# Performance work log

Hardware: AMD Instinct MI355X
Metric: run time of the kernel (lower is better)

The kernel has to match this reference:

```python
import jax, jax.numpy as jnp
import numpy as np

B, N, R = 2, 16384, 2048
CA, CS, CP, H = 128, 256, 16, 4
WQ, WK = 32, 128
NW = N // WQ
CH = CA // H
INF = 1e8


def _ln(x, w=None, b=None, eps=1e-5):
    m = jnp.mean(x, axis=-1, keepdims=True)
    v = jnp.var(x, axis=-1, keepdims=True)
    y = (x - m) * jax.lax.rsqrt(v + eps)
    if w is not None:
        y = y * w
    if b is not None:
        y = y + b
    return y


def _gather_res(x, idx):
    # x: [B, R, C], idx: [B, N] -> [B, N, C]  (torch.gather dim=1)
    return jnp.take_along_axis(x, idx[..., None], axis=1)


def _adaln(s, cond, idx, ln_w, Wg, bg, Wb):
    s = _ln(s)                      # LayerNorm, no affine
    cond = _ln(cond, ln_w)          # LayerNorm, weight only
    gate = _gather_res(cond @ Wg + bg, idx)
    bias = _gather_res(cond @ Wb, idx)
    return s * jax.nn.sigmoid(gate) + bias


def setup_inputs():
    key = jax.random.key(0)
    ks = jax.random.split(key, 20)

    def nrm(k, shape, scale=0.02):
        return jax.random.normal(k, shape, jnp.float32) * scale

    # key-window validity mask (keys are wk-wide windows centered on each wq query window)
    centers = np.arange(NW) * WQ + WQ // 2
    kidx = centers[:, None] - WK // 2 + np.arange(WK)[None, :]
    valid = (kidx >= 0) & (kidx < N)                              # [NW, WK]
    atompair_mask = jnp.broadcast_to(jnp.asarray(valid)[None, :, None, :], (B, NW, WQ, WK))

    return dict(
        atom_features=jax.random.normal(ks[0], (B, N, CA), jnp.float32),
        res_features=jax.random.normal(ks[1], (B, R, CS), jnp.float32),
        atompair_features=jax.random.normal(ks[2], (B, NW, WQ, WK, CP), jnp.float32),
        atom_res_idx=jnp.sort(jax.random.randint(ks[3], (B, N), 0, R), axis=1),
        atompos_mask=jnp.ones((B, N), jnp.float32),
        atompair_mask=atompair_mask,
        # attention AdaLN
        a_ln_w=jnp.ones((CS,), jnp.float32),
        a_Wg=nrm(ks[4], (CS, CA)), a_bg=jnp.zeros((CA,), jnp.float32), a_Wb=nrm(ks[5], (CS, CA)),
        # q / kv projections
        q_W=nrm(ks[6], (CA, CA)), q_b=jnp.zeros((CA,), jnp.float32), kv_W=nrm(ks[7], (CA, 2 * CA)),
        # pair bias head: LayerNorm(c_atompair) + Linear(c_atompair -> H, no bias)
        bij_ln_w=jnp.ones((CP,), jnp.float32), bij_ln_b=jnp.zeros((CP,), jnp.float32), bij_W=nrm(ks[8], (CP, H)),
        # residue-conditioned output gate (bias init -2)
        sg_W=nrm(ks[9], (CS, CA)), sg_b=jnp.full((CA,), -2.0, jnp.float32),
        # transition AdaLN + SwiGLU + cond gate
        t_ln_w=jnp.ones((CS,), jnp.float32),
        t_Wg=nrm(ks[10], (CS, CA)), t_bg=jnp.zeros((CA,), jnp.float32), t_Wb=nrm(ks[11], (CS, CA)),
        t_W1=nrm(ks[12], (CA, 2 * CA)), t_W2=nrm(ks[13], (CA, 2 * CA)),
        t_Wc=nrm(ks[14], (CS, CA)), t_bc=jnp.full((CA,), -2.0, jnp.float32),
        t_Wo=nrm(ks[15], (2 * CA, CA)),
    )


def reference(atom_features, res_features, atompair_features, atom_res_idx,
              atompos_mask, atompair_mask,
              a_ln_w, a_Wg, a_bg, a_Wb,
              q_W, q_b, kv_W,
              bij_ln_w, bij_ln_b, bij_W,
              sg_W, sg_b,
              t_ln_w, t_Wg, t_bg, t_Wb,
              t_W1, t_W2, t_Wc, t_bc, t_Wo):
    B_, N_ = atom_features.shape[0], atom_features.shape[1]
    # to_keys index: wk-wide key window centered on each query window (clamped; mask handles edges)
    centers = jnp.arange(NW) * WQ + WQ // 2
    kidx = jnp.clip(centers[:, None] - WK // 2 + jnp.arange(WK)[None, :], 0, N_ - 1)  # [NW, WK]

    # --- attention ---
    s = _adaln(atom_features, res_features, atom_res_idx, a_ln_w, a_Wg, a_bg, a_Wb)
    q = (s @ q_W + q_b).reshape(B_, NW, WQ, H, CH)                 # to_queries + unflatten
    kv = jnp.take(s @ kv_W, kidx, axis=1)                          # to_keys -> [B, NW, WK, 2*CA]
    kv = kv.reshape(B_, NW, WK, 2 * H, CH)
    k, v = kv[..., :H, :], kv[..., H:, :]
    a = jnp.einsum('bnqhc,bnkhc->bnqkh', q, k) / np.sqrt(CH)
    b_ij = _ln(atompair_features, bij_ln_w, bij_ln_b) @ bij_W      # [B, NW, WQ, WK, H]
    a = a + b_ij - INF * (1.0 - atompair_mask.astype(a.dtype)[..., None])
    p = jax.nn.softmax(a, axis=3)                                  # softmax over keys
    attn_out = jnp.einsum('bnqkh,bnkhc->bnqhc', p, v).reshape(B_, N_, CA)
    gate = jax.nn.sigmoid(res_features @ sg_W + sg_b)              # raw res_features (no LN)
    attn_out = attn_out * _gather_res(gate, atom_res_idx)

    atom = atom_features + attn_out * atompos_mask[..., None]

    # --- gather-conditioned transition ---
    t = _adaln(atom, res_features, atom_res_idx, t_ln_w, t_Wg, t_bg, t_Wb)
    b = jax.nn.silu(t @ t_W1) * (t @ t_W2)                          # SwiGLU, n=2
    tg = jax.nn.sigmoid(_gather_res(res_features @ t_Wc + t_bc, atom_res_idx))
    trans = tg * (b @ t_Wo)

    return atom + trans * atompos_mask[..., None]
```

## Files before the change

### kernel.cpp

```cpp
#include <hip/hip_runtime.h>
#include <hip/hip_bf16.h>
#include <string.h>

namespace {

constexpr int Bc  = 2;
constexpr int Nc  = 16384;
constexpr int Rc  = 2048;
constexpr int CAc = 128;
constexpr int CSc = 256;
constexpr int CPc = 16;
constexpr int Hc  = 4;
constexpr int WQc = 32;
constexpr int WKc = 128;
constexpr int NWc = 512;
constexpr float EPSf     = 1e-5f;
constexpr float NEG_INF  = -1e8f;
constexpr float QK_SCALE = 0.17677669529663687f;

constexpr int VT_STRIDE = 16512;
constexpr int VT_BATCH  = 128 * VT_STRIDE;

typedef short bf16x8 __attribute__((ext_vector_type(8)));
typedef float f32x4 __attribute__((ext_vector_type(4)));
typedef unsigned int u32x4 __attribute__((ext_vector_type(4)));

__device__ __forceinline__ float wsum(float v) {
#pragma unroll
  for (int m = 1; m < 64; m <<= 1) v += __shfl_xor(v, m, 64);
  return v;
}
__device__ __forceinline__ float sigm(float x) { return 1.0f / (1.0f + __expf(-x)); }
__device__ __forceinline__ float f4c(const float4& v, int i) {
  return i == 0 ? v.x : i == 1 ? v.y : i == 2 ? v.z : v.w;
}
__device__ __forceinline__ unsigned short bfx(float v) {
  __hip_bfloat16 h = __float2bfloat16(v);
  unsigned short u;
  memcpy(&u, &h, 2);
  return u;
}
__device__ __forceinline__ unsigned pk2(float a, float b) {
  return (unsigned)bfx(a) | ((unsigned)bfx(b) << 16);
}
__device__ __forceinline__ float ubf(unsigned us) {
  unsigned v = us << 16;
  float f;
  memcpy(&f, &v, 4);
  return f;
}
__device__ __forceinline__ bf16x8 ldfrag(const ushort* p) {
  return __builtin_bit_cast(bf16x8, *(const u32x4*)p);
}

__global__ void k_pack(const float* __restrict__ q_W, const float* __restrict__ kv_W,
                       const float* __restrict__ t_W1, const float* __restrict__ t_W2,
                       const float* __restrict__ t_Wo,
                       ushort* __restrict__ qWt, ushort* __restrict__ kvWt,
                       ushort* __restrict__ midWt, ushort* __restrict__ WoT,
                       ushort* __restrict__ vT) {
  const int i = blockIdx.x * 256 + threadIdx.x;
  if (i < 16384) {
    const int n = i >> 7, k = i & 127;
    qWt[i] = bfx(q_W[k * 128 + n]);
  } else if (i < 49152) {
    const int i2 = i - 16384;
    const int n = i2 >> 7, k = i2 & 127;
    kvWt[i2] = bfx(kv_W[k * 256 + n]);
  } else if (i < 114688) {
    const int i3 = i - 49152;
    const int n = i3 >> 7, k = i3 & 127;
    midWt[i3] = bfx(n < 256 ? t_W1[k * 256 + n] : t_W2[k * 256 + (n - 256)]);
  } else if (i < 147456) {
    const int i4 = i - 114688;
    const int n = i4 >> 8, k = i4 & 255;
    WoT[i4] = bfx(t_Wo[k * 128 + n]);
  } else if (i < 180224) {
    const int j = i - 147456;
    const int b = j >> 14, rem = j & 16383;
    const int d = rem >> 7, p = rem & 127;
    const int col = (p < 64) ? p : (16384 + p);
    vT[(size_t)b * VT_BATCH + (size_t)d * VT_STRIDE + col] = 0;
  }
}

__global__ void k_res_ln(const float* __restrict__ res, const float* __restrict__ a_ln_w,
                         const float* __restrict__ t_ln_w, float* __restrict__ lnA,
                         float* __restrict__ lnT) {
  const int wid = threadIdx.x >> 6, lane = threadIdx.x & 63;
  const int row = blockIdx.x * 4 + wid;
  const float* r = res + (size_t)row * CSc;
  float x[4], s = 0.f, sq = 0.f;
#pragma unroll
  for (int i = 0; i < 4; ++i) { x[i] = r[lane + 64 * i]; s += x[i]; sq += x[i] * x[i]; }
  s = wsum(s); sq = wsum(sq);
  const float mn = s * (1.0f / CSc);
  const float var = sq * (1.0f / CSc) - mn * mn;
  const float rs = rsqrtf(var + EPSf);
#pragma unroll
  for (int i = 0; i < 4; ++i) {
    const int c = lane + 64 * i;
    const float y = (x[i] - mn) * rs;
    lnA[(size_t)row * CSc + c] = y * a_ln_w[c];
    lnT[(size_t)row * CSc + c] = y * t_ln_w[c];
  }
}

__global__ void k_res_gemm(const float* __restrict__ lnA, const float* __restrict__ lnT,
                           const float* __restrict__ res,
                           const float* __restrict__ a_Wg, const float* __restrict__ a_bg,
                           const float* __restrict__ a_Wb,
                           const float* __restrict__ t_Wg, const float* __restrict__ t_bg,
                           const float* __restrict__ t_Wb,
                           const float* __restrict__ sg_W, const float* __restrict__ sg_b,
                           const float* __restrict__ t_Wc, const float* __restrict__ t_bc,
                           float* __restrict__ Ag, float* __restrict__ Ab,
                           float* __restrict__ Tg, float* __restrict__ Tb,
                           float* __restrict__ Sg, float* __restrict__ Tc) {
  __shared__ float tile[32 * CSc];
  const int m = blockIdx.y;
  const float* in = (m < 2) ? lnA : (m < 4) ? lnT : res;
  const float* W  = (m == 0) ? a_Wg : (m == 1) ? a_Wb : (m == 2) ? t_Wg
                  : (m == 3) ? t_Wb : (m == 4) ? sg_W : t_Wc;
  const float* bias = (m == 0) ? a_bg : (m == 2) ? t_bg : (m == 4) ? sg_b
                    : (m == 5) ? t_bc : nullptr;
  const bool sig = (m == 0) || (m == 2) || (m == 4) || (m == 5);
  float* out = (m == 0) ? Ag : (m == 1) ? Ab : (m == 2) ? Tg
             : (m == 3) ? Tb : (m == 4) ? Sg : Tc;
  const int row0 = blockIdx.x * 32;
  const float4* src = (const float4*)(in + (size_t)row0 * CSc);
  float4* dst = (float4*)tile;
#pragma unroll
  for (int k = 0; k < 8; ++k) dst[threadIdx.x + 256 * k] = src[threadIdx.x + 256 * k];
  __syncthreads();
  const int c0 = (threadIdx.x & 31) * 4;
  const int r0 = (threadIdx.x >> 5) * 4;
  float acc[4][4] = {};
  for (int j = 0; j < CSc; j += 4) {
    float4 a[4];
#pragma unroll
    for (int r = 0; r < 4; ++r) a[r] = *(const float4*)&tile[(r0 + r) * CSc + j];
#pragma unroll
    for (int jj = 0; jj < 4; ++jj) {
      const float4 w = *(const float4*)&W[(size_t)(j + jj) * CAc + c0];
#pragma unroll
      for (int r = 0; r < 4; ++r) {
        const float av = f4c(a[r], jj);
        acc[r][0] += av * w.x; acc[r][1] += av * w.y;
        acc[r][2] += av * w.z; acc[r][3] += av * w.w;
      }
    }
  }
  float4 bv = make_float4(0.f, 0.f, 0.f, 0.f);
  if (bias) bv = *(const float4*)&bias[c0];
#pragma unroll
  for (int r = 0; r < 4; ++r) {
    float4 o;
    o.x = acc[r][0] + bv.x; o.y = acc[r][1] + bv.y;
    o.z = acc[r][2] + bv.z; o.w = acc[r][3] + bv.w;
    if (sig) { o.x = sigm(o.x); o.y = sigm(o.y); o.z = sigm(o.z); o.w = sigm(o.w); }
    *(float4*)&out[(size_t)(row0 + r0 + r) * CAc + c0] = o;
  }
}

__global__ void k_adaln16(const float* __restrict__ in, const int* __restrict__ idxG,
                          const float* __restrict__ G, const float* __restrict__ Bb,
                          unsigned* __restrict__ out32) {
  const int wid = threadIdx.x >> 6, lane = threadIdx.x & 63;
  const int row = blockIdx.x * 4 + wid;
  const int b = row >> 14;
  const float* r = in + (size_t)row * CAc;
  const float2 xp = *(const float2*)&r[2 * lane];
  const float s = wsum(xp.x + xp.y);
  const float sq = wsum(xp.x * xp.x + xp.y * xp.y);
  const float mn = s * (1.0f / CAc);
  const float var = sq * (1.0f / CAc) - mn * mn;
  const float rs = rsqrtf(var + EPSf);
  const int base = (b * Rc + idxG[row]) * CAc;
  const float2 g2 = *(const float2*)&G[base + 2 * lane];
  const float2 b2 = *(const float2*)&Bb[base + 2 * lane];
  const float y0 = (xp.x - mn) * rs * g2.x + b2.x;
  const float y1 = (xp.y - mn) * rs * g2.y + b2.y;
  out32[(size_t)row * 64 + lane] = pk2(y0, y1);
}

__global__ __launch_bounds__(256) void k_gemm_qkv(
    const ushort* __restrict__ act16, const ushort* __restrict__ qWt,
    const ushort* __restrict__ kvWt, const float* __restrict__ q_b,
    ushort* __restrict__ q16, ushort* __restrict__ k16, ushort* __restrict__ vT) {
  __shared__ ushort vtile[128][72];
  const int ny = blockIdx.y;
  const int wid = threadIdx.x >> 6, lane = threadIdx.x & 63;
  const int c = lane & 15, s = lane >> 4;
  const int wm = wid & 1, wn = wid >> 1;
  const int base = blockIdx.x * 64;
  const int m0 = base + wm * 32;
  const int nb = wn * 64;
  const ushort* Wt = (ny == 0) ? qWt : kvWt + (ny == 2 ? 128 * 128 : 0);
  f32x4 acc[4][2];
#pragma unroll
  for (int nt = 0; nt < 4; ++nt)
#pragma unroll
    for (int mt = 0; mt < 2; ++mt) { acc[nt][mt][0]=0.f; acc[nt][mt][1]=0.f; acc[nt][mt][2]=0.f; acc[nt][mt][3]=0.f; }
#pragma unroll
  for (int kk = 0; kk < 4; ++kk) {
    const int k0 = kk * 32 + 8 * s;
    bf16x8 bA[2];
#pragma unroll
    for (int mt = 0; mt < 2; ++mt)
      bA[mt] = ldfrag(&act16[(size_t)(m0 + mt * 16 + c) * 128 + k0]);
#pragma unroll
    for (int nt = 0; nt < 4; ++nt) {
      const bf16x8 aW = ldfrag(&Wt[(size_t)(nb + nt * 16 + c) * 128 + k0]);
#pragma unroll
      for (int mt = 0; mt < 2; ++mt)
        acc[nt][mt] = __builtin_amdgcn_mfma_f32_16x16x32_bf16(aW, bA[mt], acc[nt][mt], 0, 0, 0);
    }
  }
#pragma unroll
  for (int nt = 0; nt < 4; ++nt) {
    const int colb = nb + nt * 16 + 4 * s;
    float4 qb4 = make_float4(0.f, 0.f, 0.f, 0.f);
    if (ny == 0) qb4 = *(const float4*)&q_b[colb];
#pragma unroll
    for (int mt = 0; mt < 2; ++mt) {
      const int m = m0 + mt * 16 + c;
      const f32x4 a = acc[nt][mt];
      if (ny == 0) {
        ushort4 u4;
        u4.x = bfx((a[0] + qb4.x) * QK_SCALE); u4.y = bfx((a[1] + qb4.y) * QK_SCALE);
        u4.z = bfx((a[2] + qb4.z) * QK_SCALE); u4.w = bfx((a[3] + qb4.w) * QK_SCALE);
        *(ushort4*)&q16[(size_t)m * 128 + colb] = u4;
      } else if (ny == 1) {
        ushort4 u4;
        u4.x = bfx(a[0]); u4.y = bfx(a[1]); u4.z = bfx(a[2]); u4.w = bfx(a[3]);
        *(ushort4*)&k16[(size_t)m * 128 + colb] = u4;
      } else {
        const int rowl = wm * 32 + mt * 16 + c;
#pragma unroll
        for (int r = 0; r < 4; ++r)
          vtile[colb + r][rowl] = bfx(a[r]);
      }
    }
  }
  if (ny == 2) {
    __syncthreads();
    const int bb = base >> 14, nn0 = base & 16383;
    const int t = threadIdx.x;
    const int d = t >> 1, half = t & 1;
    ushort* dst = vT + (size_t)bb * VT_BATCH + (size_t)d * VT_STRIDE + 64 + nn0 + half * 32;
    const ushort* srcl = &vtile[d][half * 32];
#pragma unroll
    for (int u = 0; u < 4; ++u)
      *(uint4*)(dst + u * 8) = *(const uint4*)(srcl + u * 8);
  }
}

__global__ __launch_bounds__(256) void k_gemm_mid(
    const ushort* __restrict__ act16, const ushort* __restrict__ midWt,
    ushort* __restrict__ bmid16) {
  const int wid = threadIdx.x >> 6, lane = threadIdx.x & 63;
  const int c = lane & 15, s = lane >> 4;
  const int wm = wid & 1, wn = wid >> 1;
  const int m0 = blockIdx.x * 64 + wm * 32;
  const int nb = blockIdx.y * 64 + wn * 32;
  f32x4 acc1[2][2], acc2[2][2];
#pragma unroll
  for (int nt = 0; nt < 2; ++nt)
#pragma unroll
    for (int mt = 0; mt < 2; ++mt) {
      acc1[nt][mt][0]=0.f; acc1[nt][mt][1]=0.f; acc1[nt][mt][2]=0.f; acc1[nt][mt][3]=0.f;
      acc2[nt][mt][0]=0.f; acc2[nt][mt][1]=0.f; acc2[nt][mt][2]=0.f; acc2[nt][mt][3]=0.f;
    }
#pragma unroll
  for (int kk = 0; kk < 4; ++kk) {
    const int k0 = kk * 32 + 8 * s;
    bf16x8 bA[2];
#pragma unroll
    for (int mt = 0; mt < 2; ++mt)
      bA[mt] = ldfrag(&act16[(size_t)(m0 + mt * 16 + c) * 128 + k0]);
#pragma unroll
    for (int nt = 0; nt < 2; ++nt) {
      const bf16x8 aW1 = ldfrag(&midWt[(size_t)(nb + nt * 16 + c) * 128 + k0]);
      const bf16x8 aW2 = ldfrag(&midWt[(size_t)(256 + nb + nt * 16 + c) * 128 + k0]);
#pragma unroll
      for (int mt = 0; mt < 2; ++mt) {
        acc1[nt][mt] = __builtin_amdgcn_mfma_f32_16x16x32_bf16(aW1, bA[mt], acc1[nt][mt], 0, 0, 0);
        acc2[nt][mt] = __builtin_amdgcn_mfma_f32_16x16x32_bf16(aW2, bA[mt], acc2[nt][mt], 0, 0, 0);
      }
    }
  }
#pragma unroll
  for (int nt = 0; nt < 2; ++nt) {
    const int colb = nb + nt * 16 + 4 * s;
#pragma unroll
    for (int mt = 0; mt < 2; ++mt) {
      const int m = m0 + mt * 16 + c;
      ushort4 u4;
#pragma unroll
      for (int r = 0; r < 4; ++r) {
        const float a1 = acc1[nt][mt][r];
        const float v = a1 * sigm(a1) * acc2[nt][mt][r];
        ((unsigned short*)&u4)[r] = bfx(v);
      }
      *(ushort4*)&bmid16[(size_t)m * 256 + colb] = u4;
    }
  }
}

__global__ __launch_bounds__(256) void k_gemm_out(
    const ushort* __restrict__ bmid16, const ushort* __restrict__ WoT,
    const float* __restrict__ atomw, const int* __restrict__ idxG,
    const float* __restrict__ TcG, const float* __restrict__ pmask,
    float* __restrict__ outG) {
  const int wid = threadIdx.x >> 6, lane = threadIdx.x & 63;
  const int c = lane & 15, s = lane >> 4;
  const int wm = wid & 1, wn = wid >> 1;
  const int m0 = blockIdx.x * 64 + wm * 32;
  const int nb = wn * 64;
  f32x4 acc[4][2];
#pragma unroll
  for (int nt = 0; nt < 4; ++nt)
#pragma unroll
    for (int mt = 0; mt < 2; ++mt) { acc[nt][mt][0]=0.f; acc[nt][mt][1]=0.f; acc[nt][mt][2]=0.f; acc[nt][mt][3]=0.f; }
#pragma unroll
  for (int kk = 0; kk < 8; ++kk) {
    const int k0 = kk * 32 + 8 * s;
    bf16x8 bA[2];
#pragma unroll
    for (int mt = 0; mt < 2; ++mt)
      bA[mt] = ldfrag(&bmid16[(size_t)(m0 + mt * 16 + c) * 256 + k0]);
#pragma unroll
    for (int nt = 0; nt < 4; ++nt) {
      const bf16x8 aW = ldfrag(&WoT[(size_t)(nb + nt * 16 + c) * 256 + k0]);
#pragma unroll
      for (int mt = 0; mt < 2; ++mt)
        acc[nt][mt] = __builtin_amdgcn_mfma_f32_16x16x32_bf16(aW, bA[mt], acc[nt][mt], 0, 0, 0);
    }
  }
#pragma unroll
  for (int mt = 0; mt < 2; ++mt) {
    const int m = m0 + mt * 16 + c;
    const int b = m >> 14;
    const int idx = idxG[m];
    const float pm = pmask[m];
    const size_t tcb = ((size_t)(b * Rc) + idx) * CAc;
#pragma unroll
    for (int nt = 0; nt < 4; ++nt) {
      const int colb = nb + nt * 16 + 4 * s;
      const float4 tc = *(const float4*)&TcG[tcb + colb];
      const float4 at = *(const float4*)&atomw[(size_t)m * CAc + colb];
      float4 o;
      o.x = at.x + tc.x * acc[nt][mt][0] * pm;
      o.y = at.y + tc.y * acc[nt][mt][1] * pm;
      o.z = at.z + tc.z * acc[nt][mt][2] * pm;
      o.w = at.w + tc.w * acc[nt][mt][3] * pm;
      *(float4*)&outG[(size_t)m * CAc + colb] = o;
    }
  }
}

__global__ __launch_bounds__(256) void k_bias2(
    const float* __restrict__ ap, const float* __restrict__ bw,
    const float* __restrict__ bb, const float* __restrict__ bW,
    ushort* __restrict__ bias16g) {
  __shared__ ushort biasL[8192];
  __shared__ float w2s[64], W2sh[4], Cbh[4];
  const int tid = threadIdx.x;
  const int bwid = blockIdx.x >> 1;
  const int half = blockIdx.x & 1;
  const int w = bwid & 511;
  if (tid < 64) w2s[tid] = bw[tid >> 2] * bW[tid];
  __syncthreads();
  if (tid < 4) {
    float a = 0.f, b2 = 0.f;
#pragma unroll
    for (int cp = 0; cp < 16; ++cp) { a += w2s[cp * 4 + tid]; b2 += bb[cp] * bW[cp * 4 + tid]; }
    W2sh[tid] = a; Cbh[tid] = b2;
  }
  __syncthreads();

  const float* apw = ap + (size_t)bwid * (WQc * WKc * CPc) + (size_t)half * (16 * 128 * CPc);
#pragma unroll
  for (int u = 0; u < 8; ++u) {
    const int p = tid + 256 * u;
    const int qql = p >> 7, kk = p & 127;
    const float* src = apw + (size_t)p * CPc;
    float sum = 0.f, sq = 0.f, d0 = 0.f, d1 = 0.f, d2 = 0.f, d3 = 0.f;
#pragma unroll
    for (int t = 0; t < 4; ++t) {
      const float4 v4 = *(const float4*)&src[t * 4];
#pragma unroll
      for (int e = 0; e < 4; ++e) {
        const float x = f4c(v4, e);
        const float4 wv = *(const float4*)&w2s[(4 * t + e) * 4];
        sum += x; sq += x * x;
        d0 += x * wv.x; d1 += x * wv.y; d2 += x * wv.z; d3 += x * wv.w;
      }
    }
    const float mn = sum * 0.0625f;
    const float var = sq * 0.0625f - mn * mn;
    const float rs = rsqrtf(var + EPSf);
    const int gk = w * 32 - 48 + kk;
    const float maskt = (gk >= 0 && gk < Nc) ? 0.f : NEG_INF;
    const int mt = kk >> 4, s_ = (kk >> 2) & 3, r_ = kk & 3;
    const int col = s_ * 16 + (qql ^ ((mt & 3) << 2) ^ s_);
    const int base = mt * 256 + col * 4 + r_;
    biasL[base]        = bfx(rs * (d0 - mn * W2sh[0]) + Cbh[0] + maskt);
    biasL[base + 2048] = bfx(rs * (d1 - mn * W2sh[1]) + Cbh[1] + maskt);
    biasL[base + 4096] = bfx(rs * (d2 - mn * W2sh[2]) + Cbh[2] + maskt);
    biasL[base + 6144] = bfx(rs * (d3 - mn * W2sh[3]) + Cbh[3] + maskt);
  }
  __syncthreads();
  uint4* dw = (uint4*)(bias16g + (size_t)bwid * 16384);
  const uint4* sl = (const uint4*)biasL;
#pragma unroll
  for (int u = 0; u < 4; ++u) {
    const int idx = tid + 256 * u;
    const int chunk = idx >> 5, within = idx & 31;
    const int h = chunk >> 3, mt = chunk & 7;
    dw[h * 512 + (mt * 2 + half) * 32 + within] = sl[idx];
  }
}

__global__ __launch_bounds__(64) void k_attn6(
    const ushort* __restrict__ qG, const ushort* __restrict__ kG,
    const ushort* __restrict__ vT, const ushort* __restrict__ bias16g,
    const int* __restrict__ idxG, const float* __restrict__ SgG,
    const float* __restrict__ pmask, const float* __restrict__ atomF,
    float* __restrict__ atomO) {
  const int bwid = blockIdx.x >> 2;
  const int h = blockIdx.x & 3;
  const int lane = threadIdx.x;
  const int c = lane & 15, s = lane >> 4;
  const int b = bwid >> 9, w = bwid & 511;
  const size_t bN = (size_t)b * Nc;

  f32x4 acc[8][2];
  {
    const ushort* bh = bias16g + (size_t)bwid * 16384 + h * 4096;
#pragma unroll
    for (int mt = 0; mt < 8; ++mt) {
      const int col = s * 16 + (c ^ ((mt & 3) << 2) ^ s);
#pragma unroll
      for (int ntq = 0; ntq < 2; ++ntq) {
        const uint2 pk = *(const uint2*)&bh[((mt * 2 + ntq) << 8) + col * 4];
        acc[mt][ntq][0] = ubf(pk.x & 0xffff);
        acc[mt][ntq][1] = ubf(pk.x >> 16);
        acc[mt][ntq][2] = ubf(pk.y & 0xffff);
        acc[mt][ntq][3] = ubf(pk.y >> 16);
      }
    }
  }

  bf16x8 bfragQ[2];
#pragma unroll
  for (int ntq = 0; ntq < 2; ++ntq) {
    const int qq = w * 32 + ntq * 16 + c;
    bfragQ[ntq] = ldfrag(&qG[(bN + qq) * CAc + h * 32 + 8 * s]);
  }
#pragma unroll
  for (int mt = 0; mt < 8; ++mt) {
    int gk = w * 32 - 48 + mt * 16 + c;
    gk = min(max(gk, 0), Nc - 1);
    const bf16x8 afragK = ldfrag(&kG[(bN + gk) * CAc + h * 32 + 8 * s]);
#pragma unroll
    for (int ntq = 0; ntq < 2; ++ntq)
      acc[mt][ntq] = __builtin_amdgcn_mfma_f32_16x16x32_bf16(afragK, bfragQ[ntq],
                                                             acc[mt][ntq], 0, 0, 0);
  }

  int ppk[8][2][2];
#pragma unroll
  for (int ntq = 0; ntq < 2; ++ntq) {
    float mx = -3e38f;
#pragma unroll
    for (int mt = 0; mt < 8; ++mt)
#pragma unroll
      for (int r = 0; r < 4; ++r) mx = fmaxf(mx, acc[mt][ntq][r]);
    mx = fmaxf(mx, __shfl_xor(mx, 16, 64));
    mx = fmaxf(mx, __shfl_xor(mx, 32, 64));
    float sm = 0.f;
#pragma unroll
    for (int mt = 0; mt < 8; ++mt)
#pragma unroll
      for (int r = 0; r < 4; ++r) {
        const float e = __expf(acc[mt][ntq][r] - mx);
        acc[mt][ntq][r] = e;
        sm += e;
      }
    sm += __shfl_xor(sm, 16, 64);
    sm += __shfl_xor(sm, 32, 64);
    const float inv = 1.0f / sm;
#pragma unroll
    for (int mt = 0; mt < 8; ++mt) {
      ppk[mt][ntq][0] = (int)pk2(acc[mt][ntq][0] * inv, acc[mt][ntq][1] * inv);
      ppk[mt][ntq][1] = (int)pk2(acc[mt][ntq][2] * inv, acc[mt][ntq][3] * inv);
    }
  }

  f32x4 opv[2][2];
#pragma unroll
  for (int i = 0; i < 2; ++i)
#pragma unroll
    for (int j = 0; j < 2; ++j) { opv[i][j][0]=0.f; opv[i][j][1]=0.f; opv[i][j][2]=0.f; opv[i][j][3]=0.f; }
  const int idxA = 4 * ((((2 * s) & 3) << 4) | c);
  const int idxB = 4 * ((((2 * s + 1) & 3) << 4) | c);
  const ushort* vTb = vT + (size_t)b * VT_BATCH;
#pragma unroll
  for (int ks = 0; ks < 4; ++ks) {
    const int vbase = 64 + w * 32 - 48 + ks * 32 + 8 * s;
    bf16x8 bV[2];
#pragma unroll
    for (int ntd = 0; ntd < 2; ++ntd) {
      const int d = h * 32 + ntd * 16 + c;
      bV[ntd] = ldfrag(&vTb[(size_t)d * VT_STRIDE + vbase]);
    }
#pragma unroll
    for (int mtp = 0; mtp < 2; ++mtp) {
      int atv[4];
      {
        const int a0 = __builtin_amdgcn_ds_bpermute(idxA, ppk[2 * ks][mtp][0]);
        const int b0 = __builtin_amdgcn_ds_bpermute(idxA, ppk[2 * ks + 1][mtp][0]);
        atv[0] = (s < 2) ? a0 : b0;
        const int a1 = __builtin_amdgcn_ds_bpermute(idxA, ppk[2 * ks][mtp][1]);
        const int b1 = __builtin_amdgcn_ds_bpermute(idxA, ppk[2 * ks + 1][mtp][1]);
        atv[1] = (s < 2) ? a1 : b1;
        const int a2 = __builtin_amdgcn_ds_bpermute(idxB, ppk[2 * ks][mtp][0]);
        const int b2 = __builtin_amdgcn_ds_bpermute(idxB, ppk[2 * ks + 1][mtp][0]);
        atv[2] = (s < 2) ? a2 : b2;
        const int a3 = __builtin_amdgcn_ds_bpermute(idxB, ppk[2 * ks][mtp][1]);
        const int b3 = __builtin_amdgcn_ds_bpermute(idxB, ppk[2 * ks + 1][mtp][1]);
        atv[3] = (s < 2) ? a3 : b3;
      }
      const bf16x8 afragP = __builtin_bit_cast(bf16x8, *(const u32x4*)atv);
#pragma unroll
      for (int ntd = 0; ntd < 2; ++ntd)
        opv[mtp][ntd] = __builtin_amdgcn_mfma_f32_16x16x32_bf16(
            afragP, bV[ntd], opv[mtp][ntd], 0, 0, 0);
    }
  }

#pragma unroll
  for (int mtp = 0; mtp < 2; ++mtp) {
#pragma unroll
    for (int r = 0; r < 4; ++r) {
      const int qq = w * 32 + mtp * 16 + 4 * s + r;
      const size_t rowg = bN + qq;
      const int residx = idxG[rowg];
      const float pm = pmask[rowg];
      const size_t gbase = ((size_t)b * Rc + residx) * CAc;
#pragma unroll
      for (int ntd = 0; ntd < 2; ++ntd) {
        const int d = h * 32 + ntd * 16 + c;
        const float g = SgG[gbase + d];
        const float af = atomF[rowg * CAc + d];
        atomO[rowg * CAc + d] = af + opv[mtp][ntd][r] * g * pm;
      }
    }
  }
}

}

extern "C" void kernel_launch(void* const* d_in, const int* in_sizes, int n_in,
                              void* d_out, int out_size, void* d_ws, size_t ws_size,
                              hipStream_t stream) {
  (void)in_sizes; (void)n_in; (void)out_size; (void)ws_size;
  const float* atomF   = (const float*)d_in[0];
  const float* resF    = (const float*)d_in[1];
  const float* apF     = (const float*)d_in[2];
  const int*   idx     = (const int*)d_in[3];
  const float* pmask   = (const float*)d_in[4];
  const float* a_ln_w  = (const float*)d_in[6];
  const float* a_Wg    = (const float*)d_in[7];
  const float* a_bg    = (const float*)d_in[8];
  const float* a_Wb    = (const float*)d_in[9];
  const float* q_W     = (const float*)d_in[10];
  const float* q_b     = (const float*)d_in[11];
  const float* kv_W    = (const float*)d_in[12];
  const float* bij_ln_w= (const float*)d_in[13];
  const float* bij_ln_b= (const float*)d_in[14];
  const float* bij_W   = (const float*)d_in[15];
  const float* sg_W    = (const float*)d_in[16];
  const float* sg_b    = (const float*)d_in[17];
  const float* t_ln_w  = (const float*)d_in[18];
  const float* t_Wg    = (const float*)d_in[19];
  const float* t_bg    = (const float*)d_in[20];
  const float* t_Wb    = (const float*)d_in[21];
  const float* t_W1    = (const float*)d_in[22];
  const float* t_W2    = (const float*)d_in[23];
  const float* t_Wc    = (const float*)d_in[24];
  const float* t_bc    = (const float*)d_in[25];
  const float* t_Wo    = (const float*)d_in[26];

  float* ws = (float*)d_ws;
  float* Ag    = ws;
  float* Ab    = Ag + 524288;
  float* Tg    = Ab + 524288;
  float* Tb    = Tg + 524288;
  float* Sg    = Tb + 524288;
  float* Tc    = Sg + 524288;
  float* lnA   = Tc + 524288;
  float* lnT   = lnA + 1048576;
  ushort* act16  = (ushort*)(lnT + 1048576);
  ushort* q16    = act16 + 4194304;
  ushort* k16    = q16 + 4194304;
  ushort* bias16g= k16 + 4194304;
  ushort* bmid16 = bias16g + 16777216;
  float* atomw   = (float*)(bmid16 + 8388608);
  ushort* qWt    = (ushort*)(atomw + 4194304);
  ushort* kvWt   = qWt + 16384;
  ushort* midWt  = kvWt + 32768;
  ushort* WoT    = midWt + 65536;
  ushort* vT     = WoT + 32768;

  k_pack<<<dim3(704), dim3(256), 0, stream>>>(q_W, kv_W, t_W1, t_W2, t_Wo,
                                              qWt, kvWt, midWt, WoT, vT);
  k_res_ln<<<dim3(Bc * Rc / 4), dim3(256), 0, stream>>>(resF, a_ln_w, t_ln_w, lnA, lnT);
  k_res_gemm<<<dim3(Bc * Rc / 32, 6), dim3(256), 0, stream>>>(
      lnA, lnT, resF, a_Wg, a_bg, a_Wb, t_Wg, t_bg, t_Wb, sg_W, sg_b, t_Wc, t_bc,
      Ag, Ab, Tg, Tb, Sg, Tc);
  k_adaln16<<<dim3(Bc * Nc / 4), dim3(256), 0, stream>>>(atomF, idx, Ag, Ab,
                                                         (unsigned*)act16);
  k_gemm_qkv<<<dim3(Bc * Nc / 64, 3), dim3(256), 0, stream>>>(act16, qWt, kvWt, q_b,
                                                              q16, k16, vT);
  k_bias2<<<dim3(Bc * NWc * 2), dim3(256), 0, stream>>>(apF, bij_ln_w, bij_ln_b, bij_W,
                                                        bias16g);
  k_attn6<<<dim3(Bc * NWc * 4), dim3(64), 0, stream>>>(q16, k16, vT, bias16g, idx, Sg,
                                                       pmask, atomF, atomw);
  k_adaln16<<<dim3(Bc * Nc / 4), dim3(256), 0, stream>>>(atomw, idx, Tg, Tb,
                                                         (unsigned*)act16);
  k_gemm_mid<<<dim3(Bc * Nc / 64, 4), dim3(256), 0, stream>>>(act16, midWt, bmid16);
  k_gemm_out<<<dim3(Bc * Nc / 64), dim3(256), 0, stream>>>(bmid16, WoT, atomw, idx, Tc,
                                                           pmask, (float*)d_out);
}
```

Before: 237.9 us.

## Fuse pair-bias computation into attention kernel and merge pack with res LayerNorm

The pair-bias kernel and the attention kernel are merged. Each 256-thread block computes the bias for half a query window into shared memory and then runs attention for 16 queries across 4 heads, one wave per head. This removes the 32 MB bf16 bias round trip through global memory and one launch. The weight pack and residue LayerNorm are also merged into one launch. In exchange, each wave now handles 16 queries instead of 32, so K and V fragments are loaded twice per window, and the bias stage's loop unroll drops to 2.

```diff
diff --git a/kernel.cpp b/kernel.cpp
--- a/kernel.cpp
+++ b/kernel.cpp
@@ -53,56 +53,57 @@
   return __builtin_bit_cast(bf16x8, *(const u32x4*)p);
 }
 
-__global__ void k_pack(const float* __restrict__ q_W, const float* __restrict__ kv_W,
-                       const float* __restrict__ t_W1, const float* __restrict__ t_W2,
-                       const float* __restrict__ t_Wo,
-                       ushort* __restrict__ qWt, ushort* __restrict__ kvWt,
-                       ushort* __restrict__ midWt, ushort* __restrict__ WoT,
-                       ushort* __restrict__ vT) {
-  const int i = blockIdx.x * 256 + threadIdx.x;
-  if (i < 16384) {
-    const int n = i >> 7, k = i & 127;
-    qWt[i] = bfx(q_W[k * 128 + n]);
-  } else if (i < 49152) {
-    const int i2 = i - 16384;
-    const int n = i2 >> 7, k = i2 & 127;
-    kvWt[i2] = bfx(kv_W[k * 256 + n]);
-  } else if (i < 114688) {
-    const int i3 = i - 49152;
-    const int n = i3 >> 7, k = i3 & 127;
-    midWt[i3] = bfx(n < 256 ? t_W1[k * 256 + n] : t_W2[k * 256 + (n - 256)]);
-  } else if (i < 147456) {
-    const int i4 = i - 114688;
-    const int n = i4 >> 8, k = i4 & 255;
-    WoT[i4] = bfx(t_Wo[k * 128 + n]);
-  } else if (i < 180224) {
-    const int j = i - 147456;
-    const int b = j >> 14, rem = j & 16383;
-    const int d = rem >> 7, p = rem & 127;
-    const int col = (p < 64) ? p : (16384 + p);
-    vT[(size_t)b * VT_BATCH + (size_t)d * VT_STRIDE + col] = 0;
-  }
-}
-
-__global__ void k_res_ln(const float* __restrict__ res, const float* __restrict__ a_ln_w,
-                         const float* __restrict__ t_ln_w, float* __restrict__ lnA,
-                         float* __restrict__ lnT) {
-  const int wid = threadIdx.x >> 6, lane = threadIdx.x & 63;
-  const int row = blockIdx.x * 4 + wid;
-  const float* r = res + (size_t)row * CSc;
-  float x[4], s = 0.f, sq = 0.f;
-#pragma unroll
-  for (int i = 0; i < 4; ++i) { x[i] = r[lane + 64 * i]; s += x[i]; sq += x[i] * x[i]; }
-  s = wsum(s); sq = wsum(sq);
-  const float mn = s * (1.0f / CSc);
-  const float var = sq * (1.0f / CSc) - mn * mn;
-  const float rs = rsqrtf(var + EPSf);
-#pragma unroll
-  for (int i = 0; i < 4; ++i) {
-    const int c = lane + 64 * i;
-    const float y = (x[i] - mn) * rs;
-    lnA[(size_t)row * CSc + c] = y * a_ln_w[c];
-    lnT[(size_t)row * CSc + c] = y * t_ln_w[c];
+__global__ void k_pack_resln(const float* __restrict__ q_W, const float* __restrict__ kv_W,
+                             const float* __restrict__ t_W1, const float* __restrict__ t_W2,
+                             const float* __restrict__ t_Wo,
+                             ushort* __restrict__ qWt, ushort* __restrict__ kvWt,
+                             ushort* __restrict__ midWt, ushort* __restrict__ WoT,
+                             ushort* __restrict__ vT,
+                             const float* __restrict__ res, const float* __restrict__ a_ln_w,
+                             const float* __restrict__ t_ln_w, float* __restrict__ lnA,
+                             float* __restrict__ lnT) {
+  if (blockIdx.x < 704) {
+    const int i = blockIdx.x * 256 + threadIdx.x;
+    if (i < 16384) {
+      const int n = i >> 7, k = i & 127;
+      qWt[i] = bfx(q_W[k * 128 + n]);
+    } else if (i < 49152) {
+      const int i2 = i - 16384;
+      const int n = i2 >> 7, k = i2 & 127;
+      kvWt[i2] = bfx(kv_W[k * 256 + n]);
+    } else if (i < 114688) {
+      const int i3 = i - 49152;
+      const int n = i3 >> 7, k = i3 & 127;
+      midWt[i3] = bfx(n < 256 ? t_W1[k * 256 + n] : t_W2[k * 256 + (n - 256)]);
+    } else if (i < 147456) {
+      const int i4 = i - 114688;
+      const int n = i4 >> 8, k = i4 & 255;
+      WoT[i4] = bfx(t_Wo[k * 128 + n]);
+    } else if (i < 180224) {
+      const int j = i - 147456;
+      const int b = j >> 14, rem = j & 16383;
+      const int d = rem >> 7, p = rem & 127;
+      const int col = (p < 64) ? p : (16384 + p);
+      vT[(size_t)b * VT_BATCH + (size_t)d * VT_STRIDE + col] = 0;
+    }
+  } else {
+    const int wid = threadIdx.x >> 6, lane = threadIdx.x & 63;
+    const int row = (blockIdx.x - 704) * 4 + wid;
+    const float* r = res + (size_t)row * CSc;
+    float x[4], s = 0.f, sq = 0.f;
+#pragma unroll
+    for (int i = 0; i < 4; ++i) { x[i] = r[lane + 64 * i]; s += x[i]; sq += x[i] * x[i]; }
+    s = wsum(s); sq = wsum(sq);
+    const float mn = s * (1.0f / CSc);
+    const float var = sq * (1.0f / CSc) - mn * mn;
+    const float rs = rsqrtf(var + EPSf);
+#pragma unroll
+    for (int i = 0; i < 4; ++i) {
+      const int c = lane + 64 * i;
+      const float y = (x[i] - mn) * rs;
+      lnA[(size_t)row * CSc + c] = y * a_ln_w[c];
+      lnT[(size_t)row * CSc + c] = y * t_ln_w[c];
+    }
   }
 }
 
@@ -245,10 +246,10 @@
   }
   if (ny == 2) {
     __syncthreads();
-    const int bb = base >> 14, nn0 = base & 16383;
+    const int bb2 = base >> 14, nn0 = base & 16383;
     const int t = threadIdx.x;
     const int d = t >> 1, half = t & 1;
-    ushort* dst = vT + (size_t)bb * VT_BATCH + (size_t)d * VT_STRIDE + 64 + nn0 + half * 32;
+    ushort* dst = vT + (size_t)bb2 * VT_BATCH + (size_t)d * VT_STRIDE + 64 + nn0 + half * 32;
     const ushort* srcl = &vtile[d][half * 32];
 #pragma unroll
     for (int u = 0; u < 4; ++u)
@@ -256,120 +257,22 @@
   }
 }
 
-__global__ __launch_bounds__(256) void k_gemm_mid(
-    const ushort* __restrict__ act16, const ushort* __restrict__ midWt,
-    ushort* __restrict__ bmid16) {
-  const int wid = threadIdx.x >> 6, lane = threadIdx.x & 63;
-  const int c = lane & 15, s = lane >> 4;
-  const int wm = wid & 1, wn = wid >> 1;
-  const int m0 = blockIdx.x * 64 + wm * 32;
-  const int nb = blockIdx.y * 64 + wn * 32;
-  f32x4 acc1[2][2], acc2[2][2];
-#pragma unroll
-  for (int nt = 0; nt < 2; ++nt)
-#pragma unroll
-    for (int mt = 0; mt < 2; ++mt) {
-      acc1[nt][mt][0]=0.f; acc1[nt][mt][1]=0.f; acc1[nt][mt][2]=0.f; acc1[nt][mt][3]=0.f;
-      acc2[nt][mt][0]=0.f; acc2[nt][mt][1]=0.f; acc2[nt][mt][2]=0.f; acc2[nt][mt][3]=0.f;
-    }
-#pragma unroll
-  for (int kk = 0; kk < 4; ++kk) {
-    const int k0 = kk * 32 + 8 * s;
-    bf16x8 bA[2];
-#pragma unroll
-    for (int mt = 0; mt < 2; ++mt)
-      bA[mt] = ldfrag(&act16[(size_t)(m0 + mt * 16 + c) * 128 + k0]);
-#pragma unroll
-    for (int nt = 0; nt < 2; ++nt) {
-      const bf16x8 aW1 = ldfrag(&midWt[(size_t)(nb + nt * 16 + c) * 128 + k0]);
-      const bf16x8 aW2 = ldfrag(&midWt[(size_t)(256 + nb + nt * 16 + c) * 128 + k0]);
-#pragma unroll
-      for (int mt = 0; mt < 2; ++mt) {
-        acc1[nt][mt] = __builtin_amdgcn_mfma_f32_16x16x32_bf16(aW1, bA[mt], acc1[nt][mt], 0, 0, 0);
-        acc2[nt][mt] = __builtin_amdgcn_mfma_f32_16x16x32_bf16(aW2, bA[mt], acc2[nt][mt], 0, 0, 0);
-      }
-    }
-  }
-#pragma unroll
-  for (int nt = 0; nt < 2; ++nt) {
-    const int colb = nb + nt * 16 + 4 * s;
-#pragma unroll
-    for (int mt = 0; mt < 2; ++mt) {
-      const int m = m0 + mt * 16 + c;
-      ushort4 u4;
-#pragma unroll
-      for (int r = 0; r < 4; ++r) {
-        const float a1 = acc1[nt][mt][r];
-        const float v = a1 * sigm(a1) * acc2[nt][mt][r];
-        ((unsigned short*)&u4)[r] = bfx(v);
-      }
-      *(ushort4*)&bmid16[(size_t)m * 256 + colb] = u4;
-    }
-  }
-}
-
-__global__ __launch_bounds__(256) void k_gemm_out(
-    const ushort* __restrict__ bmid16, const ushort* __restrict__ WoT,
-    const float* __restrict__ atomw, const int* __restrict__ idxG,
-    const float* __restrict__ TcG, const float* __restrict__ pmask,
-    float* __restrict__ outG) {
-  const int wid = threadIdx.x >> 6, lane = threadIdx.x & 63;
-  const int c = lane & 15, s = lane >> 4;
-  const int wm = wid & 1, wn = wid >> 1;
-  const int m0 = blockIdx.x * 64 + wm * 32;
-  const int nb = wn * 64;
-  f32x4 acc[4][2];
-#pragma unroll
-  for (int nt = 0; nt < 4; ++nt)
-#pragma unroll
-    for (int mt = 0; mt < 2; ++mt) { acc[nt][mt][0]=0.f; acc[nt][mt][1]=0.f; acc[nt][mt][2]=0.f; acc[nt][mt][3]=0.f; }
-#pragma unroll
-  for (int kk = 0; kk < 8; ++kk) {
-    const int k0 = kk * 32 + 8 * s;
-    bf16x8 bA[2];
-#pragma unroll
-    for (int mt = 0; mt < 2; ++mt)
-      bA[mt] = ldfrag(&bmid16[(size_t)(m0 + mt * 16 + c) * 256 + k0]);
-#pragma unroll
-    for (int nt = 0; nt < 4; ++nt) {
-      const bf16x8 aW = ldfrag(&WoT[(size_t)(nb + nt * 16 + c) * 256 + k0]);
-#pragma unroll
-      for (int mt = 0; mt < 2; ++mt)
-        acc[nt][mt] = __builtin_amdgcn_mfma_f32_16x16x32_bf16(aW, bA[mt], acc[nt][mt], 0, 0, 0);
-    }
-  }
-#pragma unroll
-  for (int mt = 0; mt < 2; ++mt) {
-    const int m = m0 + mt * 16 + c;
-    const int b = m >> 14;
-    const int idx = idxG[m];
-    const float pm = pmask[m];
-    const size_t tcb = ((size_t)(b * Rc) + idx) * CAc;
-#pragma unroll
-    for (int nt = 0; nt < 4; ++nt) {
-      const int colb = nb + nt * 16 + 4 * s;
-      const float4 tc = *(const float4*)&TcG[tcb + colb];
-      const float4 at = *(const float4*)&atomw[(size_t)m * CAc + colb];
-      float4 o;
-      o.x = at.x + tc.x * acc[nt][mt][0] * pm;
-      o.y = at.y + tc.y * acc[nt][mt][1] * pm;
-      o.z = at.z + tc.z * acc[nt][mt][2] * pm;
-      o.w = at.w + tc.w * acc[nt][mt][3] * pm;
-      *(float4*)&outG[(size_t)m * CAc + colb] = o;
-    }
-  }
-}
-
-__global__ __launch_bounds__(256) void k_bias2(
+__global__ __launch_bounds__(256) void k_battn(
     const float* __restrict__ ap, const float* __restrict__ bw,
     const float* __restrict__ bb, const float* __restrict__ bW,
-    ushort* __restrict__ bias16g) {
+    const ushort* __restrict__ qG, const ushort* __restrict__ kG,
+    const ushort* __restrict__ vT,
+    const int* __restrict__ idxG, const float* __restrict__ SgG,
+    const float* __restrict__ pmask, const float* __restrict__ atomF,
+    float* __restrict__ atomO) {
   __shared__ ushort biasL[8192];
   __shared__ float w2s[64], W2sh[4], Cbh[4];
   const int tid = threadIdx.x;
   const int bwid = blockIdx.x >> 1;
   const int half = blockIdx.x & 1;
-  const int w = bwid & 511;
+  const int b = bwid >> 9, w = bwid & 511;
+  const size_t bN = (size_t)b * Nc;
+
   if (tid < 64) w2s[tid] = bw[tid >> 2] * bW[tid];
   __syncthreads();
   if (tid < 4) {
@@ -379,9 +282,8 @@
     W2sh[tid] = a; Cbh[tid] = b2;
   }
   __syncthreads();
-
   const float* apw = ap + (size_t)bwid * (WQc * WKc * CPc) + (size_t)half * (16 * 128 * CPc);
-#pragma unroll
+#pragma unroll 2
   for (int u = 0; u < 8; ++u) {
     const int p = tid + 256 * u;
     const int qql = p >> 7, kk = p & 127;
@@ -412,72 +314,42 @@
     biasL[base + 6144] = bfx(rs * (d3 - mn * W2sh[3]) + Cbh[3] + maskt);
   }
   __syncthreads();
-  uint4* dw = (uint4*)(bias16g + (size_t)bwid * 16384);
-  const uint4* sl = (const uint4*)biasL;
-#pragma unroll
-  for (int u = 0; u < 4; ++u) {
-    const int idx = tid + 256 * u;
-    const int chunk = idx >> 5, within = idx & 31;
-    const int h = chunk >> 3, mt = chunk & 7;
-    dw[h * 512 + (mt * 2 + half) * 32 + within] = sl[idx];
-  }
-}
-
-__global__ __launch_bounds__(64) void k_attn6(
-    const ushort* __restrict__ qG, const ushort* __restrict__ kG,
-    const ushort* __restrict__ vT, const ushort* __restrict__ bias16g,
-    const int* __restrict__ idxG, const float* __restrict__ SgG,
-    const float* __restrict__ pmask, const float* __restrict__ atomF,
-    float* __restrict__ atomO) {
-  const int bwid = blockIdx.x >> 2;
-  const int h = blockIdx.x & 3;
-  const int lane = threadIdx.x;
+
+  const int h = tid >> 6;
+  const int lane = tid & 63;
   const int c = lane & 15, s = lane >> 4;
-  const int b = bwid >> 9, w = bwid & 511;
-  const size_t bN = (size_t)b * Nc;
-
-  f32x4 acc[8][2];
+
+  f32x4 acc[8];
   {
-    const ushort* bh = bias16g + (size_t)bwid * 16384 + h * 4096;
+    const ushort* bh = &biasL[h * 2048];
 #pragma unroll
     for (int mt = 0; mt < 8; ++mt) {
       const int col = s * 16 + (c ^ ((mt & 3) << 2) ^ s);
-#pragma unroll
-      for (int ntq = 0; ntq < 2; ++ntq) {
-        const uint2 pk = *(const uint2*)&bh[((mt * 2 + ntq) << 8) + col * 4];
-        acc[mt][ntq][0] = ubf(pk.x & 0xffff);
-        acc[mt][ntq][1] = ubf(pk.x >> 16);
-        acc[mt][ntq][2] = ubf(pk.y & 0xffff);
-        acc[mt][ntq][3] = ubf(pk.y >> 16);
-      }
-    }
-  }
-
-  bf16x8 bfragQ[2];
-#pragma unroll
-  for (int ntq = 0; ntq < 2; ++ntq) {
-    const int qq = w * 32 + ntq * 16 + c;
-    bfragQ[ntq] = ldfrag(&qG[(bN + qq) * CAc + h * 32 + 8 * s]);
-  }
+      const uint2 pk = *(const uint2*)&bh[mt * 256 + col * 4];
+      acc[mt][0] = ubf(pk.x & 0xffff);
+      acc[mt][1] = ubf(pk.x >> 16);
+      acc[mt][2] = ubf(pk.y & 0xffff);
+      acc[mt][3] = ubf(pk.y >> 16);
+    }
+  }
+
+  const int qq = w * 32 + half * 16 + c;
+  const bf16x8 bfragQ = ldfrag(&qG[(bN + qq) * CAc + h * 32 + 8 * s]);
 #pragma unroll
   for (int mt = 0; mt < 8; ++mt) {
     int gk = w * 32 - 48 + mt * 16 + c;
     gk = min(max(gk, 0), Nc - 1);
     const bf16x8 afragK = ldfrag(&kG[(bN + gk) * CAc + h * 32 + 8 * s]);
-#pragma unroll
-    for (int ntq = 0; ntq < 2; ++ntq)
-      acc[mt][ntq] = __builtin_amdgcn_mfma_f32_16x16x32_bf16(afragK, bfragQ[ntq],
-                                                             acc[mt][ntq], 0, 0, 0);
-  }
-
-  int ppk[8][2][2];
-#pragma unroll
-  for (int ntq = 0; ntq < 2; ++ntq) {
+    acc[mt] = __builtin_amdgcn_mfma_f32_16x16x32_bf16(afragK, bfragQ, acc[mt], 0, 0, 0);
+  }
+
+  int ppk[8][2];
+  {
     float mx = -3e38f;
 #pragma unroll
     for (int mt = 0; mt < 8; ++mt)
 #pragma unroll
-      for (int r = 0; r < 4; ++r) mx = fmaxf(mx, acc[mt][ntq][r]);
+      for (int r = 0; r < 4; ++r) mx = fmaxf(mx, acc[mt][r]);
     mx = fmaxf(mx, __shfl_xor(mx, 16, 64));
     mx = fmaxf(mx, __shfl_xor(mx, 32, 64));
     float sm = 0.f;
@@ -485,8 +357,8 @@
     for (int mt = 0; mt < 8; ++mt)
 #pragma unroll
       for (int r = 0; r < 4; ++r) {
-        const float e = __expf(acc[mt][ntq][r] - mx);
-        acc[mt][ntq][r] = e;
+        const float e = __expf(acc[mt][r] - mx);
+        acc[mt][r] = e;
         sm += e;
       }
     sm += __shfl_xor(sm, 16, 64);
@@ -494,16 +366,14 @@
     const float inv = 1.0f / sm;
 #pragma unroll
     for (int mt = 0; mt < 8; ++mt) {
-      ppk[mt][ntq][0] = (int)pk2(acc[mt][ntq][0] * inv, acc[mt][ntq][1] * inv);
-      ppk[mt][ntq][1] = (int)pk2(acc[mt][ntq][2] * inv, acc[mt][ntq][3] * inv);
-    }
-  }
-
-  f32x4 opv[2][2];
-#pragma unroll
-  for (int i = 0; i < 2; ++i)
-#pragma unroll
-    for (int j = 0; j < 2; ++j) { opv[i][j][0]=0.f; opv[i][j][1]=0.f; opv[i][j][2]=0.f; opv[i][j][3]=0.f; }
+      ppk[mt][0] = (int)pk2(acc[mt][0] * inv, acc[mt][1] * inv);
+      ppk[mt][1] = (int)pk2(acc[mt][2] * inv, acc[mt][3] * inv);
+    }
+  }
+
+  f32x4 opv[2];
+  opv[0][0]=0.f; opv[0][1]=0.f; opv[0][2]=0.f; opv[0][3]=0.f;
+  opv[1][0]=0.f; opv[1][1]=0.f; opv[1][2]=0.f; opv[1][3]=0.f;
   const int idxA = 4 * ((((2 * s) & 3) << 4) | c);
   const int idxB = 4 * ((((2 * s + 1) & 3) << 4) | c);
   const ushort* vTb = vT + (size_t)b * VT_BATCH;
@@ -516,47 +386,144 @@
       const int d = h * 32 + ntd * 16 + c;
       bV[ntd] = ldfrag(&vTb[(size_t)d * VT_STRIDE + vbase]);
     }
-#pragma unroll
-    for (int mtp = 0; mtp < 2; ++mtp) {
-      int atv[4];
-      {
-        const int a0 = __builtin_amdgcn_ds_bpermute(idxA, ppk[2 * ks][mtp][0]);
-        const int b0 = __builtin_amdgcn_ds_bpermute(idxA, ppk[2 * ks + 1][mtp][0]);
-        atv[0] = (s < 2) ? a0 : b0;
-        const int a1 = __builtin_amdgcn_ds_bpermute(idxA, ppk[2 * ks][mtp][1]);
-        const int b1 = __builtin_amdgcn_ds_bpermute(idxA, ppk[2 * ks + 1][mtp][1]);
-        atv[1] = (s < 2) ? a1 : b1;
-        const int a2 = __builtin_amdgcn_ds_bpermute(idxB, ppk[2 * ks][mtp][0]);
-        const int b2 = __builtin_amdgcn_ds_bpermute(idxB, ppk[2 * ks + 1][mtp][0]);
-        atv[2] = (s < 2) ? a2 : b2;
-        const int a3 = __builtin_amdgcn_ds_bpermute(idxB, ppk[2 * ks][mtp][1]);
-        const int b3 = __builtin_amdgcn_ds_bpermute(idxB, ppk[2 * ks + 1][mtp][1]);
-        atv[3] = (s < 2) ? a3 : b3;
+    int atv[4];
+    {
+      const int a0 = __builtin_amdgcn_ds_bpermute(idxA, ppk[2 * ks][0]);
+      const int b0 = __builtin_amdgcn_ds_bpermute(idxA, ppk[2 * ks + 1][0]);
+      atv[0] = (s < 2) ? a0 : b0;
+      const int a1 = __builtin_amdgcn_ds_bpermute(idxA, ppk[2 * ks][1]);
+      const int b1 = __builtin_amdgcn_ds_bpermute(idxA, ppk[2 * ks + 1][1]);
+      atv[1] = (s < 2) ? a1 : b1;
+      const int a2 = __builtin_amdgcn_ds_bpermute(idxB, ppk[2 * ks][0]);
+      const int b2 = __builtin_amdgcn_ds_bpermute(idxB, ppk[2 * ks + 1][0]);
+      atv[2] = (s < 2) ? a2 : b2;
+      const int a3 = __builtin_amdgcn_ds_bpermute(idxB, ppk[2 * ks][1]);
+      const int b3 = __builtin_amdgcn_ds_bpermute(idxB, ppk[2 * ks + 1][1]);
+      atv[3] = (s < 2) ? a3 : b3;
+    }
+    const bf16x8 afragP = __builtin_bit_cast(bf16x8, *(const u32x4*)atv);
+#pragma unroll
+    for (int ntd = 0; ntd < 2; ++ntd)
+      opv[ntd] = __builtin_amdgcn_mfma_f32_16x16x32_bf16(afragP, bV[ntd], opv[ntd], 0, 0, 0);
+  }
+
+#pragma unroll
+  for (int r = 0; r < 4; ++r) {
+    const int qr = w * 32 + half * 16 + 4 * s + r;
+    const size_t rowg = bN + qr;
+    const int residx = idxG[rowg];
+    const float pm = pmask[rowg];
+    const size_t gbase = ((size_t)b * Rc + residx) * CAc;
+#pragma unroll
+    for (int ntd = 0; ntd < 2; ++ntd) {
+      const int d = h * 32 + ntd * 16 + c;
+      const float g = SgG[gbase + d];
+      const float af = atomF[rowg * CAc + d];
+      atomO[rowg * CAc + d] = af + opv[ntd][r] * g * pm;
+    }
+  }
+}
+
+__global__ __launch_bounds__(256) void k_gemm_mid(
+    const ushort* __restrict__ act16, const ushort* __restrict__ midWt,
+    ushort* __restrict__ bmid16) {
+  const int wid = threadIdx.x >> 6, lane = threadIdx.x & 63;
+  const int c = lane & 15, s = lane >> 4;
+  const int wm = wid & 1, wn = wid >> 1;
+  const int m0 = blockIdx.x * 64 + wm * 32;
+  const int nb = blockIdx.y * 64 + wn * 32;
+  f32x4 acc1[2][2], acc2[2][2];
+#pragma unroll
+  for (int nt = 0; nt < 2; ++nt)
+#pragma unroll
+    for (int mt = 0; mt < 2; ++mt) {
+      acc1[nt][mt][0]=0.f; acc1[nt][mt][1]=0.f; acc1[nt][mt][2]=0.f; acc1[nt][mt][3]=0.f;
+      acc2[nt][mt][0]=0.f; acc2[nt][mt][1]=0.f; acc2[nt][mt][2]=0.f; acc2[nt][mt][3]=0.f;
+    }
+#pragma unroll
+  for (int kk = 0; kk < 4; ++kk) {
+    const int k0 = kk * 32 + 8 * s;
+    bf16x8 bA[2];
+#pragma unroll
+    for (int mt = 0; mt < 2; ++mt)
+      bA[mt] = ldfrag(&act16[(size_t)(m0 + mt * 16 + c) * 128 + k0]);
+#pragma unroll
+    for (int nt = 0; nt < 2; ++nt) {
+      const bf16x8 aW1 = ldfrag(&midWt[(size_t)(nb + nt * 16 + c) * 128 + k0]);
+      const bf16x8 aW2 = ldfrag(&midWt[(size_t)(256 + nb + nt * 16 + c) * 128 + k0]);
+#pragma unroll
+      for (int mt = 0; mt < 2; ++mt) {
+        acc1[nt][mt] = __builtin_amdgcn_mfma_f32_16x16x32_bf16(aW1, bA[mt], acc1[nt][mt], 0, 0, 0);
+        acc2[nt][mt] = __builtin_amdgcn_mfma_f32_16x16x32_bf16(aW2, bA[mt], acc2[nt][mt], 0, 0, 0);
       }
-      const bf16x8 afragP = __builtin_bit_cast(bf16x8, *(const u32x4*)atv);
-#pragma unroll
-      for (int ntd = 0; ntd < 2; ++ntd)
-        opv[mtp][ntd] = __builtin_amdgcn_mfma_f32_16x16x32_bf16(
-            afragP, bV[ntd], opv[mtp][ntd], 0, 0, 0);
-    }
-  }
-
-#pragma unroll
-  for (int mtp = 0; mtp < 2; ++mtp) {
-#pragma unroll
-    for (int r = 0; r < 4; ++r) {
-      const int qq = w * 32 + mtp * 16 + 4 * s + r;
-      const size_t rowg = bN + qq;
-      const int residx = idxG[rowg];
-      const float pm = pmask[rowg];
-      const size_t gbase = ((size_t)b * Rc + residx) * CAc;
-#pragma unroll
-      for (int ntd = 0; ntd < 2; ++ntd) {
-        const int d = h * 32 + ntd * 16 + c;
-        const float g = SgG[gbase + d];
-        const float af = atomF[rowg * CAc + d];
-        atomO[rowg * CAc + d] = af + opv[mtp][ntd][r] * g * pm;
+    }
+  }
+#pragma unroll
+  for (int nt = 0; nt < 2; ++nt) {
+    const int colb = nb + nt * 16 + 4 * s;
+#pragma unroll
+    for (int mt = 0; mt < 2; ++mt) {
+      const int m = m0 + mt * 16 + c;
+      ushort4 u4;
+#pragma unroll
+      for (int r = 0; r < 4; ++r) {
+        const float a1 = acc1[nt][mt][r];
+        const float v = a1 * sigm(a1) * acc2[nt][mt][r];
+        ((unsigned short*)&u4)[r] = bfx(v);
       }
+      *(ushort4*)&bmid16[(size_t)m * 256 + colb] = u4;
+    }
+  }
+}
+
+__global__ __launch_bounds__(256) void k_gemm_out(
+    const ushort* __restrict__ bmid16, const ushort* __restrict__ WoT,
+    const float* __restrict__ atomw, const int* __restrict__ idxG,
+    const float* __restrict__ TcG, const float* __restrict__ pmask,
+    float* __restrict__ outG) {
+  const int wid = threadIdx.x >> 6, lane = threadIdx.x & 63;
+  const int c = lane & 15, s = lane >> 4;
+  const int wm = wid & 1, wn = wid >> 1;
+  const int m0 = blockIdx.x * 64 + wm * 32;
+  const int nb = wn * 64;
+  f32x4 acc[4][2];
+#pragma unroll
+  for (int nt = 0; nt < 4; ++nt)
+#pragma unroll
+    for (int mt = 0; mt < 2; ++mt) { acc[nt][mt][0]=0.f; acc[nt][mt][1]=0.f; acc[nt][mt][2]=0.f; acc[nt][mt][3]=0.f; }
+#pragma unroll
+  for (int kk = 0; kk < 8; ++kk) {
+    const int k0 = kk * 32 + 8 * s;
+    bf16x8 bA[2];
+#pragma unroll
+    for (int mt = 0; mt < 2; ++mt)
+      bA[mt] = ldfrag(&bmid16[(size_t)(m0 + mt * 16 + c) * 256 + k0]);
+#pragma unroll
+    for (int nt = 0; nt < 4; ++nt) {
+      const bf16x8 aW = ldfrag(&WoT[(size_t)(nb + nt * 16 + c) * 256 + k0]);
+#pragma unroll
+      for (int mt = 0; mt < 2; ++mt)
+        acc[nt][mt] = __builtin_amdgcn_mfma_f32_16x16x32_bf16(aW, bA[mt], acc[nt][mt], 0, 0, 0);
+    }
+  }
+#pragma unroll
+  for (int mt = 0; mt < 2; ++mt) {
+    const int m = m0 + mt * 16 + c;
+    const int b = m >> 14;
+    const int idx = idxG[m];
+    const float pm = pmask[m];
+    const size_t tcb = ((size_t)(b * Rc) + idx) * CAc;
+#pragma unroll
+    for (int nt = 0; nt < 4; ++nt) {
+      const int colb = nb + nt * 16 + 4 * s;
+      const float4 tc = *(const float4*)&TcG[tcb + colb];
+      const float4 at = *(const float4*)&atomw[(size_t)m * CAc + colb];
+      float4 o;
+      o.x = at.x + tc.x * acc[nt][mt][0] * pm;
+      o.y = at.y + tc.y * acc[nt][mt][1] * pm;
+      o.z = at.z + tc.z * acc[nt][mt][2] * pm;
+      o.w = at.w + tc.w * acc[nt][mt][3] * pm;
+      *(float4*)&outG[(size_t)m * CAc + colb] = o;
     }
   }
 }
@@ -606,8 +573,7 @@
   ushort* act16  = (ushort*)(lnT + 1048576);
   ushort* q16    = act16 + 4194304;
   ushort* k16    = q16 + 4194304;
-  ushort* bias16g= k16 + 4194304;
-  ushort* bmid16 = bias16g + 16777216;
+  ushort* bmid16 = k16 + 4194304;
   float* atomw   = (float*)(bmid16 + 8388608);
   ushort* qWt    = (ushort*)(atomw + 4194304);
   ushort* kvWt   = qWt + 16384;
@@ -615,9 +581,9 @@
   ushort* WoT    = midWt + 65536;
   ushort* vT     = WoT + 32768;
 
-  k_pack<<<dim3(704), dim3(256), 0, stream>>>(q_W, kv_W, t_W1, t_W2, t_Wo,
-                                              qWt, kvWt, midWt, WoT, vT);
-  k_res_ln<<<dim3(Bc * Rc / 4), dim3(256), 0, stream>>>(resF, a_ln_w, t_ln_w, lnA, lnT);
+  k_pack_resln<<<dim3(1728), dim3(256), 0, stream>>>(
+      q_W, kv_W, t_W1, t_W2, t_Wo, qWt, kvWt, midWt, WoT, vT,
+      resF, a_ln_w, t_ln_w, lnA, lnT);
   k_res_gemm<<<dim3(Bc * Rc / 32, 6), dim3(256), 0, stream>>>(
       lnA, lnT, resF, a_Wg, a_bg, a_Wb, t_Wg, t_bg, t_Wb, sg_W, sg_b, t_Wc, t_bc,
       Ag, Ab, Tg, Tb, Sg, Tc);
@@ -625,10 +591,8 @@
                                                          (unsigned*)act16);
   k_gemm_qkv<<<dim3(Bc * Nc / 64, 3), dim3(256), 0, stream>>>(act16, qWt, kvWt, q_b,
                                                               q16, k16, vT);
-  k_bias2<<<dim3(Bc * NWc * 2), dim3(256), 0, stream>>>(apF, bij_ln_w, bij_ln_b, bij_W,
-                                                        bias16g);
-  k_attn6<<<dim3(Bc * NWc * 4), dim3(64), 0, stream>>>(q16, k16, vT, bias16g, idx, Sg,
-                                                       pmask, atomF, atomw);
+  k_battn<<<dim3(Bc * NWc * 2), dim3(256), 0, stream>>>(
+      apF, bij_ln_w, bij_ln_b, bij_W, q16, k16, vT, idx, Sg, pmask, atomF, atomw);
   k_adaln16<<<dim3(Bc * Nc / 4), dim3(256), 0, stream>>>(atomw, idx, Tg, Tb,
                                                          (unsigned*)act16);
   k_gemm_mid<<<dim3(Bc * Nc / 64, 4), dim3(256), 0, stream>>>(act16, midWt, bmid16);
```

Measured after the change: 218.2 us. 1.09x faster.
